# Performance work log

Hardware: AMD Instinct MI355X
Metric: run time of the kernel (lower is better)

Reference implementation:

```python
import jax, jax.numpy as jnp
import numpy as np

WS = 8          # attention window size
NUM_HEADS = 4
PATCH_RATIO = 2 # ratio between consecutive pyramid levels
SCALES = 3


def _rel_idx(ws):
    ch = np.arange(ws)
    coords = np.stack(np.meshgrid(ch, ch, indexing='ij')).reshape(2, -1)
    rel = (coords[:, :, None] - coords[:, None, :]).transpose(1, 2, 0)
    rel[:, :, 0] += ws - 1
    rel[:, :, 1] += ws - 1
    rel[:, :, 0] *= 2 * ws - 1
    return jnp.asarray(rel.sum(-1))  # [ws*ws, ws*ws] int

REL_IDX = _rel_idx(WS)


def win_part(x, ws):
    B, H, W, C = x.shape
    x = x.reshape(B, H // ws, ws, W // ws, ws, C).transpose(0, 1, 3, 2, 4, 5)
    return x.reshape(-1, ws, ws, C)


def win_rev(w, ws, B, H, W):
    C = w.shape[-1]
    x = w.reshape(B, H // ws, W // ws, ws, ws, C).transpose(0, 1, 3, 2, 4, 5)
    return x.reshape(B, H, W, C)


def cross_attn(xw, yw, mw, qw, qb, kw, kb, vw, vb, pw, pb, table):
    # xw, yw: [Bn, N, C]; mw: [Bn, N] overexposure mask
    Bn, N, C = xw.shape
    hd = C // NUM_HEADS
    scale = hd ** -0.5
    q = (xw @ qw.T + qb).reshape(Bn, N, NUM_HEADS, hd).transpose(0, 2, 1, 3) * scale
    k = (yw @ kw.T + kb).reshape(Bn, N, NUM_HEADS, hd).transpose(0, 2, 1, 3)
    v = (yw @ vw.T + vb).reshape(Bn, N, NUM_HEADS, hd).transpose(0, 2, 1, 3)
    attn = jnp.einsum('bhnd,bhmd->bhnm', q, k)
    mask_attn = mw[:, None, :] * mw[:, :, None]          # [Bn, N, N]
    attn = attn * mask_attn[:, None]                     # multiplicative exposure mask
    bias = table[REL_IDX]                                # [N, N, heads]
    attn = attn + bias.transpose(2, 0, 1)[None]
    attn = jax.nn.softmax(attn, axis=-1)
    out = jnp.einsum('bhnm,bhmd->bhnd', attn, v).transpose(0, 2, 1, 3).reshape(Bn, N, C)
    out = out @ pw.T + pb
    return out, attn


def align_level(x, y, params):
    # x, y: [B, H, W, C]; shift_size = 0 (module default)
    B, H, W, C = x.shape
    mask = jnp.where(x > 0.95, 0.0, 1.0).mean(-1, keepdims=True)  # [B,H,W,1]
    x = x * mask
    xw = win_part(x, WS).reshape(-1, WS * WS, C)
    yw = win_part(y, WS).reshape(-1, WS * WS, C)
    mw = win_part(mask, WS).reshape(-1, WS * WS)
    out, attn = cross_attn(xw, yw, mw, *params)
    out = win_rev(out.reshape(-1, WS, WS, C), WS, B, H, W)
    return out, attn


def atttransfer(ta, att, pr):
    # ta: [B, H, W, C] at finer level; att: [nW, heads, WS^2, WS^2] from coarser level
    B, H, W, C = ta.shape
    ws = WS * pr
    w = win_part(ta, ws)                                  # [nW, ws, ws, C]
    nW = w.shape[0]
    w = w.reshape(nW, WS, pr, WS, pr, C).transpose(0, 1, 3, 2, 4, 5)
    w = w.reshape(nW, WS * WS, pr * pr * C)
    out = att.mean(axis=1) @ w                            # [nW, WS^2, pr^2*C]
    out = out.reshape(nW, WS, WS, pr, pr, C).transpose(0, 1, 3, 2, 4, 5).reshape(nW, ws, ws, C)
    return win_rev(out, ws, B, H, W)


def conv3(x, w, b):
    y = jax.lax.conv_general_dilated(x, w, (1, 1), 'SAME',
                                     dimension_numbers=('NCHW', 'OIHW', 'NCHW'))
    return y + b[None, :, None, None]


def lrelu(x):
    return jax.nn.leaky_relu(x, 0.1)


def _forward(ref1, ref2, ref3, ta1, ta2, ta3, q_w, q_b, k_w, k_b, v_w, v_b,
             p_w, p_b, bias_table, fc_w, fc_b):
    refs = [ref1, ref2, ref3]
    tas = [ta1, ta2, ta3]
    upsample_feat = None
    last_att = None
    feat = None
    for i in range(SCALES, 0, -1):
        j = i - 1
        ref = refs[j].transpose(0, 2, 3, 1)   # NCHW -> NHWC
        ta = tas[j].transpose(0, 2, 3, 1)
        params = (q_w[j], q_b[j], k_w[j], k_b[j], v_w[j], v_b[j],
                  p_w[j], p_b[j], bias_table[j])
        aligned, att = align_level(ref, ta, params)
        feat = aligned.transpose(0, 3, 1, 2)  # NHWC -> NCHW
        if i < SCALES:
            atrans = atttransfer(ta, last_att, PATCH_RATIO).transpose(0, 3, 1, 2)
            feat = conv3(jnp.concatenate([feat, upsample_feat, atrans], axis=1),
                         fc_w[j], fc_b[j])
        if i > 1:
            feat = lrelu(feat)
            B, C, Hh, Ww = feat.shape
            upsample_feat = jax.image.resize(feat, (B, C, Hh * 2, Ww * 2), method='bilinear')
        last_att = att
    return lrelu(feat)


def setup_inputs() -> dict:
    key = jax.random.key(0)
    ks = jax.random.split(key, 20)
    B, C = 4, 64
    d = {}
    d['ref1'] = jax.random.normal(ks[0], (B, C, 256, 256), jnp.float32)
    d['ref2'] = jax.random.normal(ks[1], (B, C, 128, 128), jnp.float32)
    d['ref3'] = jax.random.normal(ks[2], (B, C, 64, 64), jnp.float32)
    d['ta1'] = jax.random.normal(ks[3], (B, C, 256, 256), jnp.float32)
    d['ta2'] = jax.random.normal(ks[4], (B, C, 128, 128), jnp.float32)
    d['ta3'] = jax.random.normal(ks[5], (B, C, 64, 64), jnp.float32)
    d['q_w'] = jax.random.normal(ks[6], (3, C, C), jnp.float32) * 0.02
    d['q_b'] = jax.random.normal(ks[7], (3, C), jnp.float32) * 0.02
    d['k_w'] = jax.random.normal(ks[8], (3, C, C), jnp.float32) * 0.02
    d['k_b'] = jax.random.normal(ks[9], (3, C), jnp.float32) * 0.02
    d['v_w'] = jax.random.normal(ks[10], (3, C, C), jnp.float32) * 0.02
    d['v_b'] = jax.random.normal(ks[11], (3, C), jnp.float32) * 0.02
    d['p_w'] = jax.random.normal(ks[12], (3, C, C), jnp.float32) * 0.02
    d['p_b'] = jax.random.normal(ks[13], (3, C), jnp.float32) * 0.02
    d['bias_table'] = jax.random.normal(ks[14], (3, (2 * WS - 1) ** 2, NUM_HEADS), jnp.float32) * 0.02
    d['fc_w'] = jax.random.normal(ks[15], (2, C, 3 * C, 3, 3), jnp.float32) * 0.02
    d['fc_b'] = jax.random.normal(ks[16], (2, C), jnp.float32) * 0.02
    return d


def reference(ref1, ref2, ref3, ta1, ta2, ta3, q_w, q_b, k_w, k_b, v_w, v_b,
              p_w, p_b, bias_table, fc_w, fc_b):
    return _forward(ref1, ref2, ref3, ta1, ta2, ta3, q_w, q_b, k_w, k_b,
                    v_w, v_b, p_w, p_b, bias_table, fc_w, fc_b)
```

## Files before the change

kernel.cpp:

```cpp
#include <hip/hip_runtime.h>
#include <hip/hip_bf16.h>
#include <math.h>

#define LRELU(v) ((v) >= 0.f ? (v) : 0.1f * (v))
#define LOG2E 1.4426950408889634f

typedef __attribute__((ext_vector_type(8))) short short8;
typedef __attribute__((ext_vector_type(4))) float f32x4;

#define MFMA16 __builtin_amdgcn_mfma_f32_16x16x32_bf16

__device__ __forceinline__ float loadf(const float* p) { return *p; }
__device__ __forceinline__ float loadf(const __hip_bfloat16* p) { return __bfloat162float(*p); }
__device__ __forceinline__ short f2bfbits(float f) {
    __hip_bfloat16 h = __float2bfloat16(f);
    return *reinterpret_cast<short*>(&h);
}
__device__ __forceinline__ float bits2f(unsigned short u) {
    union { unsigned int i; float f; } x; x.i = ((unsigned int)u) << 16; return x.f;
}

__global__ __launch_bounds__(256) void nhwc_kernel(const float* __restrict__ ref,
                                                   const float* __restrict__ ta,
                                                   __hip_bfloat16* __restrict__ refn,
                                                   __hip_bfloat16* __restrict__ tan,
                                                   float* __restrict__ maskp,
                                                   int H, int HW) {
    __shared__ float S[2][64][67];
    const int tid = threadIdx.x;
    const int tile = blockIdx.x;
    const int b = blockIdx.y;
    const int tpr = H >> 6;
    const int y = tile / tpr;
    const int x0 = (tile - y * tpr) << 6;
    const size_t ibase = (size_t)b * 64 * HW + (size_t)y * H + x0;

    for (int r = tid; r < 8192; r += 256) {
        int which = r >> 12;
        int c = (r >> 6) & 63;
        int x = r & 63;
        S[which][c][x] = (which ? ta : ref)[ibase + (size_t)c * HW + x];
    }
    __syncthreads();
    if (tid < 64) {
        float s = 0.f;
#pragma unroll
        for (int c = 0; c < 64; ++c) s += (S[0][c][tid] > 0.95f) ? 0.f : 1.f;
        maskp[(size_t)b * HW + (size_t)y * H + x0 + tid] = s * (1.f / 64.f);
    }
    const size_t obase = ((size_t)b * HW + (size_t)y * H + x0) * 64;
    for (int r = tid; r < 8192; r += 256) {
        int which = r >> 12;
        int x = (r >> 6) & 63;
        int c = r & 63;
        (which ? tan : refn)[obase + (size_t)x * 64 + c] = __float2bfloat16(S[which][c][x]);
    }
}

template <bool HASATT>
__global__ __launch_bounds__(256, 4) void fused_attn_kernel(
    const __hip_bfloat16* __restrict__ refn,
    const __hip_bfloat16* __restrict__ tan,
    const float* __restrict__ maskp,
    const __hip_bfloat16* __restrict__ WQ,
    const __hip_bfloat16* __restrict__ WK,
    const __hip_bfloat16* __restrict__ WV,
    const __hip_bfloat16* __restrict__ WPp,
    const float* __restrict__ qb, const float* __restrict__ kb,
    const float* __restrict__ vb, const float* __restrict__ pb,
    const float* __restrict__ btab,
    __hip_bfloat16* __restrict__ aligned,
    __hip_bfloat16* __restrict__ attm,
    int H, int nWx, int nWin)
{
    __shared__ __align__(16) unsigned short PP[64 * 72];
    __shared__ __align__(16) unsigned short KH[64 * 72];
    __shared__ __align__(16) unsigned short VT[64 * 72];
    __shared__ unsigned short BLB[900];
    __shared__ float MSK[64];

    const int HW = H * H;
    const int win = blockIdx.x;
    const int bb = blockIdx.y;
    const int wy = win / nWx, wx = win - wy * nWx;
    const int y0 = wy * 8, x0 = wx * 8;
    const int tid = threadIdx.x;
    const int w = __builtin_amdgcn_readfirstlane(tid >> 6);
    const int l = tid & 63;
    const int lq = l >> 4, lm = l & 15;

    for (int r = tid; r < 900; r += 256)
        BLB[r] = (unsigned short)f2bfbits(btab[r] * LOG2E);
    if (tid < 64)
        MSK[tid] = maskp[(size_t)bb * HW + (size_t)(y0 + (tid >> 3)) * H + x0 + (tid & 7)];

    const int tokr = 16 * w + lm;
    const size_t prow = ((size_t)bb * HW
                         + (size_t)(y0 + (tokr >> 3)) * H + (x0 + (tokr & 7))) * 64;
    const unsigned short* xp = (const unsigned short*)refn + prow;
    const unsigned short* yp = (const unsigned short*)tan + prow;

    f32x4 aq[4], ak[4], av[4];
#pragma unroll
    for (int nt = 0; nt < 4; ++nt) {
        aq[nt] = (f32x4){0.f, 0.f, 0.f, 0.f};
        ak[nt] = (f32x4){0.f, 0.f, 0.f, 0.f};
        av[nt] = (f32x4){0.f, 0.f, 0.f, 0.f};
    }

#pragma unroll
    for (int stage = 0; stage < 2; ++stage) {
        const int cio = stage * 32 + lq * 8;
        short8 xa = *reinterpret_cast<const short8*>(xp + cio);
        short8 ya = *reinterpret_cast<const short8*>(yp + cio);
#pragma unroll
        for (int nt = 0; nt < 4; ++nt) {
            const int co = nt * 16 + lm;
            short8 bq = *reinterpret_cast<const short8*>(WQ + co * 64 + cio);
            aq[nt] = MFMA16(xa, bq, aq[nt], 0, 0, 0);
            short8 bk = *reinterpret_cast<const short8*>(WK + co * 64 + cio);
            ak[nt] = MFMA16(ya, bk, ak[nt], 0, 0, 0);
            short8 bv8 = *reinterpret_cast<const short8*>(WV + co * 64 + cio);
            av[nt] = MFMA16(ya, bv8, av[nt], 0, 0, 0);
        }
    }

#pragma unroll
    for (int nt = 0; nt < 4; ++nt) {
        const int co = nt * 16 + lm;
        const float kbv = kb[co], vbv = vb[co];
#pragma unroll
        for (int r = 0; r < 4; ++r) {
            const int tr = 16 * w + lq * 4 + r;
            const int pr = 16 * (2 * (tr >> 5) + ((tr >> 2) & 1))
                         + 4 * ((tr >> 3) & 3) + (tr & 3);
            KH[pr * 72 + co] = (unsigned short)f2bfbits(ak[nt][r] + kbv);
            VT[co * 72 + tr] = (unsigned short)f2bfbits(av[nt][r] + vbv);
        }
    }
    {
        float mq_r[4];
#pragma unroll
        for (int r = 0; r < 4; ++r) mq_r[r] = MSK[16 * w + lq * 4 + r];
#pragma unroll
        for (int nt = 0; nt < 4; ++nt) {
            const float qbv = qb[nt * 16 + lm];
#pragma unroll
            for (int r = 0; r < 4; ++r)
                PP[(16 * w + lq * 4 + r) * 72 + nt * 16 + lm] =
                    (unsigned short)f2bfbits((aq[nt][r] * mq_r[r] + qbv) * 0.25f);
        }
    }
    __syncthreads();

    const short8 z8 = (short8){0, 0, 0, 0, 0, 0, 0, 0};
    const f32x4 zf = (f32x4){0.f, 0.f, 0.f, 0.f};
    short8 qfrag[4];
#pragma unroll
    for (int h = 0; h < 4; ++h)
        qfrag[h] = (lq < 2)
            ? *reinterpret_cast<const short8*>(&PP[(16 * w + lm) * 72 + 16 * h + lq * 8])
            : z8;

    const float mql = MSK[16 * w + lm] * LOG2E;
    float mkb[4][4];
    int ktab[4][4];
#pragma unroll
    for (int nt = 0; nt < 4; ++nt)
#pragma unroll
        for (int r = 0; r < 4; ++r) {
            int kt = (nt >> 1) * 32 + lq * 8 + (nt & 1) * 4 + r;
            ktab[nt][r] = kt;
            mkb[nt][r] = MSK[kt];
        }
    const int qt = 16 * w + lm;
    const int qi = qt >> 3, qj = qt & 7;

    float attAcc[HASATT ? 4 : 1][HASATT ? 4 : 1];
    if constexpr (HASATT) {
#pragma unroll
        for (int nt = 0; nt < 4; ++nt)
#pragma unroll
            for (int r = 0; r < 4; ++r) attAcc[nt][r] = 0.f;
    }
    f32x4 oacc[4];

#pragma unroll
    for (int hp = 0; hp < 2; ++hp) {
        f32x4 s[2][4];
#pragma unroll
        for (int u = 0; u < 2; ++u) {
            const int h = hp * 2 + u;
#pragma unroll
            for (int nt = 0; nt < 4; ++nt) {
                short8 kf = (lq < 2)
                    ? *reinterpret_cast<const short8*>(
                          &KH[(nt * 16 + lm) * 72 + 16 * h + lq * 8])
                    : z8;
                s[u][nt] = MFMA16(kf, qfrag[h], zf, 0, 0, 0);
            }
        }

        float p[2][4][4];
#pragma unroll
        for (int u = 0; u < 2; ++u) {
            const int h = hp * 2 + u;
#pragma unroll
            for (int nt = 0; nt < 4; ++nt)
#pragma unroll
                for (int r = 0; r < 4; ++r) {
                    int kt = ktab[nt][r];
                    int bidx = (qi - (kt >> 3) + 7) * 15 + (qj - (kt & 7) + 7);
                    p[u][nt][r] = s[u][nt][r] * mql * mkb[nt][r]
                                  + bits2f(BLB[bidx * 4 + h]);
                }
        }
        float mx[2], sum[2];
#pragma unroll
        for (int u = 0; u < 2; ++u) {
            float m = p[u][0][0];
#pragma unroll
            for (int nt = 0; nt < 4; ++nt)
#pragma unroll
                for (int r = 0; r < 4; ++r) m = fmaxf(m, p[u][nt][r]);
            m = fmaxf(m, __shfl_xor(m, 16));
            m = fmaxf(m, __shfl_xor(m, 32));
            mx[u] = m;
        }
#pragma unroll
        for (int u = 0; u < 2; ++u) {
            float sm = 0.f;
#pragma unroll
            for (int nt = 0; nt < 4; ++nt)
#pragma unroll
                for (int r = 0; r < 4; ++r) {
                    p[u][nt][r] = exp2f(p[u][nt][r] - mx[u]);
                    sm += p[u][nt][r];
                }
            sm += __shfl_xor(sm, 16);
            sm += __shfl_xor(sm, 32);
            sum[u] = sm;
        }
#pragma unroll
        for (int u = 0; u < 2; ++u) {
            float inv = 1.f / sum[u];
#pragma unroll
            for (int nt = 0; nt < 4; ++nt)
#pragma unroll
                for (int r = 0; r < 4; ++r) p[u][nt][r] *= inv;
        }

        if constexpr (HASATT) {
#pragma unroll
            for (int u = 0; u < 2; ++u)
#pragma unroll
                for (int nt = 0; nt < 4; ++nt)
#pragma unroll
                    for (int r = 0; r < 4; ++r) attAcc[nt][r] += 0.25f * p[u][nt][r];
        }

#pragma unroll
        for (int u = 0; u < 2; ++u) {
            const int h = hp * 2 + u;
            short8 pb0, pb1;
#pragma unroll
            for (int j = 0; j < 8; ++j) {
                pb0[j] = f2bfbits(p[u][(j >> 2)][j & 3]);
                pb1[j] = f2bfbits(p[u][2 + (j >> 2)][j & 3]);
            }
            short8 vt0 = *reinterpret_cast<const short8*>(&VT[(16 * h + lm) * 72 + lq * 8]);
            short8 vt1 = *reinterpret_cast<const short8*>(&VT[(16 * h + lm) * 72 + 32 + lq * 8]);
            f32x4 o = MFMA16(vt0, pb0, zf, 0, 0, 0);
            o = MFMA16(vt1, pb1, o, 0, 0, 0);
            oacc[h] = o;
        }
    }

    if constexpr (HASATT) {
#pragma unroll
        for (int nt = 0; nt < 4; ++nt)
#pragma unroll
            for (int r = 0; r < 4; ++r)
                PP[(16 * w + lm) * 72 + ktab[nt][r]] =
                    (unsigned short)f2bfbits(attAcc[nt][r]);
        const int rr = 16 * w + (l >> 2), cb = (l & 3) * 16;
        short8 a0 = *reinterpret_cast<const short8*>(&PP[rr * 72 + cb]);
        short8 a1 = *reinterpret_cast<const short8*>(&PP[rr * 72 + cb + 8]);
        unsigned short* gp = (unsigned short*)attm
            + ((size_t)bb * nWin + win) * 4096 + (size_t)rr * 64 + cb;
        *reinterpret_cast<short8*>(gp) = a0;
        *reinterpret_cast<short8*>(gp + 8) = a1;
    }

    short8 oa0, oa1;
#pragma unroll
    for (int j = 0; j < 8; ++j) {
        oa0[j] = f2bfbits(oacc[(j >> 2)][j & 3]);
        oa1[j] = f2bfbits(oacc[2 + (j >> 2)][j & 3]);
    }
    f32x4 eo[4];
#pragma unroll
    for (int nt = 0; nt < 4; ++nt) {
        const int co = nt * 16 + lm;
        short8 wb0 = *reinterpret_cast<const short8*>(WPp + co * 64 + lq * 8);
        short8 wb1 = *reinterpret_cast<const short8*>(WPp + co * 64 + 32 + lq * 8);
        eo[nt] = MFMA16(oa0, wb0, zf, 0, 0, 0);
        eo[nt] = MFMA16(oa1, wb1, eo[nt], 0, 0, 0);
    }
    const size_t obase = (size_t)bb * HW * 64;
#pragma unroll
    for (int nt = 0; nt < 4; ++nt) {
        float pbv = pb[nt * 16 + lm];
#pragma unroll
        for (int r = 0; r < 4; ++r) {
            int tok = 16 * w + lq * 4 + r;
            aligned[obase + ((size_t)(y0 + (tok >> 3)) * H + (x0 + (tok & 7))) * 64
                    + nt * 16 + lm] = __float2bfloat16(eo[nt][r] + pbv);
        }
    }
}

__global__ __launch_bounds__(256) void wsplit_kernel(const float* __restrict__ qw,
                                                     const float* __restrict__ kw,
                                                     const float* __restrict__ vw,
                                                     const float* __restrict__ pw,
                                                     __hip_bfloat16* __restrict__ dst) {
    int idx = blockIdx.x * 256 + threadIdx.x;
    int e = idx & 4095;
    int mat = (idx >> 12) & 3;
    int j = idx >> 14;
    int co = e >> 6, ci = e & 63;
    int src_ci = ci;
    if (mat == 3)
        src_ci = 16 * (2 * (ci >> 5) + ((ci >> 2) & 1)) + 4 * ((ci >> 3) & 3) + (ci & 3);
    const float* src = (mat == 0 ? qw : mat == 1 ? kw : mat == 2 ? vw : pw) + j * 4096;
    float v = src[co * 64 + src_ci];
    __hip_bfloat16 h = __float2bfloat16(v);
    dst[((size_t)j * 4 + mat) * 8192 + e] = h;
    dst[((size_t)j * 4 + mat) * 8192 + 4096 + e] = __float2bfloat16(v - __bfloat162float(h));
}

#define PSTR 4624
__global__ __launch_bounds__(256) void atttrans_kernel(
    const __hip_bfloat16* __restrict__ tan,
    const __hip_bfloat16* __restrict__ attm,
    __hip_bfloat16* __restrict__ outw,
    int H, int HW, int nWx16)
{
    __shared__ __align__(16) unsigned short AT[4608];
    __shared__ __align__(16) unsigned short VTP[4 * PSTR];

    const int tid = threadIdx.x;
    const int win = blockIdx.x;
    const int b = blockIdx.y;
    const int wh = win / nWx16, ww = win - wh * nWx16;
    const int w = __builtin_amdgcn_readfirstlane(tid >> 6);
    const int l = tid & 63;
    const int lq = l >> 4, lm = l & 15;

    const unsigned short* ap = (const unsigned short*)attm
        + ((size_t)b * nWx16 * nWx16 + win) * 4096;
    for (int s = tid; s < 512; s += 256) {
        short8 v = *reinterpret_cast<const short8*>(ap + s * 8);
        *reinterpret_cast<short8*>(&AT[(s >> 3) * 72 + (s & 7) * 8]) = v;
    }

    {
        const int yy = tid >> 4, xx = tid & 15;
        const int pp = ((yy & 1) << 1) | (xx & 1);
        const int s = ((yy >> 1) << 3) | (xx >> 1);
        const unsigned short* tp = (const unsigned short*)tan
            + ((size_t)b * HW + (size_t)(wh * 16 + yy) * H + (ww * 16 + xx)) * 64;
        unsigned short* vbp = &VTP[pp * PSTR + s];
#pragma unroll
        for (int oct = 0; oct < 8; ++oct) {
            short8 v = *reinterpret_cast<const short8*>(tp + oct * 8);
#pragma unroll
            for (int i = 0; i < 8; ++i) vbp[(oct * 8 + i) * 72] = (unsigned short)v[i];
        }
    }
    __syncthreads();

    f32x4 acc[4][4];
#pragma unroll
    for (int pp = 0; pp < 4; ++pp)
#pragma unroll
        for (int nt = 0; nt < 4; ++nt) acc[pp][nt] = (f32x4){0.f, 0.f, 0.f, 0.f};

#pragma unroll
    for (int kk = 0; kk < 2; ++kk) {
        short8 aA = *reinterpret_cast<const short8*>(
                        &AT[(16 * w + lm) * 72 + kk * 32 + lq * 8]);
#pragma unroll
        for (int pp = 0; pp < 4; ++pp) {
#pragma unroll
            for (int nt = 0; nt < 4; ++nt) {
                short8 bB = *reinterpret_cast<const short8*>(
                    &VTP[pp * PSTR + (nt * 16 + lm) * 72 + kk * 32 + lq * 8]);
                acc[pp][nt] = MFMA16(aA, bB, acc[pp][nt], 0, 0, 0);
            }
        }
    }

#pragma unroll
    for (int pp = 0; pp < 4; ++pp) {
        const int pi = pp >> 1, pj = pp & 1;
#pragma unroll
        for (int r = 0; r < 4; ++r) {
            const int t = 16 * w + lq * 4 + r;
            const int Y = wh * 16 + ((t >> 3) << 1) + pi;
            const int X = ww * 16 + ((t & 7) << 1) + pj;
            __hip_bfloat16* op = outw + ((size_t)b * HW + (size_t)Y * H + X) * 64;
#pragma unroll
            for (int nt = 0; nt < 4; ++nt)
                op[nt * 16 + lm] = __float2bfloat16(acc[pp][nt][r]);
        }
    }
}

__global__ __launch_bounds__(256) void wtrans_kernel(const float* __restrict__ src,
                                                     __hip_bfloat16* __restrict__ WH,
                                                     __hip_bfloat16* __restrict__ WL) {
    int idx = blockIdx.x * 256 + threadIdx.x;
    int j = idx & 7;
    int t1 = idx >> 3;
    int co = t1 & 63;
    int t2 = t1 >> 6;
    int oct = t2 & 3;
    int t3 = t2 >> 2;
    int chunk = t3 % 6;
    int kykx = t3 / 6;
    int ci = chunk * 32 + oct * 8 + j;
    int ky = kykx / 3, kx = kykx % 3;
    float v = src[((co * 192 + ci) * 3 + ky) * 3 + kx];
    __hip_bfloat16 h = __float2bfloat16(v);
    WH[idx] = h;
    WL[idx] = __float2bfloat16(v - __bfloat162float(h));
}

__global__ __launch_bounds__(256) void conv_mfma_kernel(
    const __hip_bfloat16* __restrict__ s0, const __hip_bfloat16* __restrict__ s1,
    const __hip_bfloat16* __restrict__ s2,
    const __hip_bfloat16* __restrict__ WHp,
    const float* __restrict__ bias,
    float* __restrict__ out,
    int H, int HW, int mode)
{
    __shared__ short I[6][66][40];

    const int tid = threadIdx.x;
    const int w   = tid >> 6;
    const int l   = tid & 63;
    const int lq  = l >> 4;
    const int lm  = l & 15;
    const int x0  = blockIdx.x * 64;
    const int y0  = blockIdx.y * 4;
    const size_t zoff = (size_t)blockIdx.z * HW * 64;

    f32x4 acc[4][4];
#pragma unroll
    for (int mt = 0; mt < 4; ++mt)
#pragma unroll
        for (int nt = 0; nt < 4; ++nt) acc[mt][nt] = (f32x4){0.f, 0.f, 0.f, 0.f};

    const short8* WH8 = reinterpret_cast<const short8*>(WHp);

    for (int chunk = 0; chunk < 6; ++chunk) {
        __syncthreads();
        const unsigned short* src = reinterpret_cast<const unsigned short*>(
            (chunk < 2) ? s0 : (chunk < 4) ? s1 : s2);
        const int cib = (chunk & 1) * 32;
        for (int s = tid; s < 1584; s += 256) {
            int oct = s & 3;
            int xr = s >> 2;
            int xi = xr % 66;
            int r = xr / 66;
            int gx = x0 - 1 + xi, gy = y0 - 1 + r;
            short8 v = (short8){0, 0, 0, 0, 0, 0, 0, 0};
            if (gx >= 0 && gx < H && gy >= 0 && gy < H)
                v = *reinterpret_cast<const short8*>(
                        src + zoff + ((size_t)gy * H + gx) * 64 + cib + oct * 8);
            *reinterpret_cast<short8*>(&I[r][xi][oct * 8]) = v;
        }
        __syncthreads();

#pragma unroll
        for (int kk = 0; kk < 9; ++kk) {
            const int ky = kk / 3, kx = kk % 3;
            const int wbase = ((kk * 6 + chunk) * 4 + lq) * 64 + lm;
            short8 ah[4];
#pragma unroll
            for (int mt = 0; mt < 4; ++mt) ah[mt] = WH8[wbase + mt * 16];
#pragma unroll
            for (int nt = 0; nt < 4; ++nt) {
                short8 bfrag = *reinterpret_cast<const short8*>(
                                   &I[w + ky][nt * 16 + lm + kx][lq * 8]);
#pragma unroll
                for (int mt = 0; mt < 4; ++mt)
                    acc[mt][nt] = MFMA16(ah[mt], bfrag, acc[mt][nt], 0, 0, 0);
            }
        }
    }

    const int y = y0 + w;
#pragma unroll
    for (int mt = 0; mt < 4; ++mt) {
#pragma unroll
        for (int r = 0; r < 4; ++r) {
            const int co = mt * 16 + lq * 4 + r;
            const float bv = bias[co];
#pragma unroll
            for (int nt = 0; nt < 4; ++nt) {
                float v = acc[mt][nt][r] + bv;
                const int x = x0 + nt * 16 + lm;
                if (mode == 0) {
                    v = LRELU(v);
                    out[zoff + (size_t)co * HW + (size_t)y * H + x] = v;
                } else {
                    out[zoff + ((size_t)y * H + x) * 64 + co] = v;
                }
            }
        }
    }
}

template <typename T>
__global__ __launch_bounds__(256) void upsample_kernel(const T* __restrict__ in,
                                                       __hip_bfloat16* __restrict__ out,
                                                       int Hin, int total) {
    int idx = blockIdx.x * 256 + threadIdx.x;
    if (idx >= total) return;
    int c = idx & 63;
    int r1 = idx >> 6;
    int W2 = Hin * 2;
    int X = r1 % W2;
    int r2 = r1 / W2;
    int Y = r2 % W2;
    int b = r2 / W2;
    int y0 = Y >> 1, x0 = X >> 1;
    int ya = (Y & 1) ? y0 + 1 : y0 - 1;
    int xa = (X & 1) ? x0 + 1 : x0 - 1;
    ya = ya < 0 ? 0 : (ya >= Hin ? Hin - 1 : ya);
    xa = xa < 0 ? 0 : (xa >= Hin ? Hin - 1 : xa);
    const T* p = in + (size_t)b * Hin * Hin * 64;
    float v00 = LRELU(loadf(p + ((size_t)y0 * Hin + x0) * 64 + c));
    float v01 = LRELU(loadf(p + ((size_t)y0 * Hin + xa) * 64 + c));
    float v10 = LRELU(loadf(p + ((size_t)ya * Hin + x0) * 64 + c));
    float v11 = LRELU(loadf(p + ((size_t)ya * Hin + xa) * 64 + c));
    out[idx] = __float2bfloat16(0.5625f * v00 + 0.1875f * (v01 + v10) + 0.0625f * v11);
}

extern "C" void kernel_launch(void* const* d_in, const int* in_sizes, int n_in,
                              void* d_out, int out_size, void* d_ws, size_t ws_size,
                              hipStream_t stream) {
    const float* refs[3] = { (const float*)d_in[0], (const float*)d_in[1], (const float*)d_in[2] };
    const float* tas[3]  = { (const float*)d_in[3], (const float*)d_in[4], (const float*)d_in[5] };
    const float* q_w = (const float*)d_in[6];
    const float* q_b = (const float*)d_in[7];
    const float* k_w = (const float*)d_in[8];
    const float* k_b = (const float*)d_in[9];
    const float* v_w = (const float*)d_in[10];
    const float* v_b = (const float*)d_in[11];
    const float* p_w = (const float*)d_in[12];
    const float* p_b = (const float*)d_in[13];
    const float* btab = (const float*)d_in[14];
    const float* fc_w = (const float*)d_in[15];
    const float* fc_b = (const float*)d_in[16];

    const size_t WBYTES = 4ull * 221184 + 196608;
    const size_t BIG4 = 4ull * 65536 * 64 * 2;
    const size_t NEED4 = WBYTES + 4 * BIG4 + 4ull * 65536 * 4 + 4096;
    const int NB = (ws_size >= NEED4) ? 4 : 1;
    const size_t BIG = (size_t)NB * 65536 * 64 * 2;

    char* p = (char*)d_ws;
    __hip_bfloat16* WH0 = (__hip_bfloat16*)p;  p += 221184;
    __hip_bfloat16* WL0 = (__hip_bfloat16*)p;  p += 221184;
    __hip_bfloat16* WH1 = (__hip_bfloat16*)p;  p += 221184;
    __hip_bfloat16* WL1 = (__hip_bfloat16*)p;  p += 221184;
    __hip_bfloat16* WTA = (__hip_bfloat16*)p;  p += 196608;
    __hip_bfloat16* XRN = (__hip_bfloat16*)p;  p += BIG;
    __hip_bfloat16* XTN = (__hip_bfloat16*)p;  p += BIG;
    __hip_bfloat16* ALIGNED = (__hip_bfloat16*)p;  p += BIG;
    __hip_bfloat16* UPS     = (__hip_bfloat16*)p;  p += BIG;
    float* MASKP = (float*)p;  p += (size_t)NB * 65536 * 4;
    __hip_bfloat16* ATRANS = XRN;
    __hip_bfloat16 *ATTMA, *ATTMB;
    float* FEAT2;
    if (NB == 4) {
        ATTMA = (__hip_bfloat16*)d_out;
        ATTMB = (__hip_bfloat16*)((float*)d_out + 1048576);
        FEAT2 = (float*)d_out + 5242880;
    } else {
        ATTMA = (__hip_bfloat16*)p;  p += (size_t)64 * 4096 * 2;
        ATTMB = (__hip_bfloat16*)p;  p += (size_t)256 * 4096 * 2;
        FEAT2 = (float*)p;           p += (size_t)16384 * 64 * 4;
    }

    wtrans_kernel<<<432, 256, 0, stream>>>(fc_w, WH0, WL0);
    wtrans_kernel<<<432, 256, 0, stream>>>(fc_w + 110592, WH1, WL1);
    wsplit_kernel<<<192, 256, 0, stream>>>(q_w, k_w, v_w, p_w, WTA);

    for (int b0 = 0; b0 < 4; b0 += NB) {
        const float* ref1 = refs[0] + (size_t)b0 * 64 * 65536;
        const float* ta1  = tas[0]  + (size_t)b0 * 64 * 65536;
        const float* ref2 = refs[1] + (size_t)b0 * 64 * 16384;
        const float* ta2  = tas[1]  + (size_t)b0 * 64 * 16384;
        const float* ref3 = refs[2] + (size_t)b0 * 64 * 4096;
        const float* ta3  = tas[2]  + (size_t)b0 * 64 * 4096;

        nhwc_kernel<<<dim3(64, NB), 256, 0, stream>>>(ref3, ta3, XRN, XTN, MASKP, 64, 4096);
        fused_attn_kernel<true><<<dim3(64, NB), 256, 0, stream>>>(
            XRN, XTN, MASKP,
            WTA + (2*4+0)*8192, WTA + (2*4+1)*8192, WTA + (2*4+2)*8192, WTA + (2*4+3)*8192,
            q_b + 2*64, k_b + 2*64, v_b + 2*64, p_b + 2*64,
            btab + 2*900, ALIGNED, ATTMA, 64, 8, 64);
        upsample_kernel<__hip_bfloat16><<<(NB * 64 * 16384) / 256, 256, 0, stream>>>(
            ALIGNED, UPS, 64, NB * 64 * 16384);

        nhwc_kernel<<<dim3(256, NB), 256, 0, stream>>>(ref2, ta2, XRN, XTN, MASKP, 128, 16384);
        fused_attn_kernel<true><<<dim3(256, NB), 256, 0, stream>>>(
            XRN, XTN, MASKP,
            WTA + (1*4+0)*8192, WTA + (1*4+1)*8192, WTA + (1*4+2)*8192, WTA + (1*4+3)*8192,
            q_b + 64, k_b + 64, v_b + 64, p_b + 64,
            btab + 900, ALIGNED, ATTMB, 128, 16, 256);
        atttrans_kernel<<<dim3(64, NB), 256, 0, stream>>>(
            XTN, ATTMA, ATRANS, 128, 16384, 8);
        conv_mfma_kernel<<<dim3(2, 32, NB), 256, 0, stream>>>(
            ALIGNED, UPS, ATRANS, WH1, fc_b + 64, FEAT2, 128, 16384, 1);
        upsample_kernel<float><<<(NB * 64 * 65536) / 256, 256, 0, stream>>>(
            FEAT2, UPS, 128, NB * 64 * 65536);

        nhwc_kernel<<<dim3(1024, NB), 256, 0, stream>>>(ref1, ta1, XRN, XTN, MASKP, 256, 65536);
        fused_attn_kernel<false><<<dim3(1024, NB), 256, 0, stream>>>(
            XRN, XTN, MASKP,
            WTA + 0*8192, WTA + 1*8192, WTA + 2*8192, WTA + 3*8192,
            q_b, k_b, v_b, p_b,
            btab, ALIGNED, nullptr, 256, 32, 1024);
        atttrans_kernel<<<dim3(256, NB), 256, 0, stream>>>(
            XTN, ATTMB, ATRANS, 256, 65536, 16);
        conv_mfma_kernel<<<dim3(4, 64, NB), 256, 0, stream>>>(
            ALIGNED, UPS, ATRANS, WH0, fc_b,
            (float*)d_out + (size_t)b0 * 64 * 65536, 256, 65536, 0);
    }
}
```

Before: 431.2 us.

## Prefetch next conv input chunk into registers while computing current chunk

```diff
diff --git a/kernel.cpp b/kernel.cpp
--- a/kernel.cpp
+++ b/kernel.cpp
@@ -456,6 +456,7 @@
     const int x0  = blockIdx.x * 64;
     const int y0  = blockIdx.y * 4;
     const size_t zoff = (size_t)blockIdx.z * HW * 64;
+    const short8 z8 = (short8){0, 0, 0, 0, 0, 0, 0, 0};
 
     f32x4 acc[4][4];
 #pragma unroll
@@ -465,25 +466,51 @@
 
     const short8* WH8 = reinterpret_cast<const short8*>(WHp);
 
+    short8 st[7];
+    const unsigned short* b0 = (const unsigned short*)s0;
+    const unsigned short* b1 = (const unsigned short*)s1;
+    const unsigned short* b2 = (const unsigned short*)s2;
+
+    auto stage_load = [&](int chunk) {
+        const unsigned short* src = (chunk < 2) ? b0 : (chunk < 4) ? b1 : b2;
+        const int cib = (chunk & 1) * 32;
+#pragma unroll
+        for (int s = 0; s < 7; ++s) {
+            int slot = tid + (s << 8);
+            if (slot < 1584) {
+                int oct = slot & 3;
+                int xr = slot >> 2;
+                int xi = xr % 66;
+                int r = xr / 66;
+                int gx = x0 - 1 + xi, gy = y0 - 1 + r;
+                short8 v = z8;
+                if (gx >= 0 && gx < H && gy >= 0 && gy < H)
+                    v = *reinterpret_cast<const short8*>(
+                            src + zoff + ((size_t)gy * H + gx) * 64 + cib + oct * 8);
+                st[s] = v;
+            }
+        }
+    };
+    auto stage_write = [&]() {
+#pragma unroll
+        for (int s = 0; s < 7; ++s) {
+            int slot = tid + (s << 8);
+            if (slot < 1584) {
+                int oct = slot & 3;
+                int xr = slot >> 2;
+                int xi = xr % 66;
+                int r = xr / 66;
+                *reinterpret_cast<short8*>(&I[r][xi][oct * 8]) = st[s];
+            }
+        }
+    };
+
+    stage_load(0);
+    stage_write();
+    __syncthreads();
+
     for (int chunk = 0; chunk < 6; ++chunk) {
-        __syncthreads();
-        const unsigned short* src = reinterpret_cast<const unsigned short*>(
-            (chunk < 2) ? s0 : (chunk < 4) ? s1 : s2);
-        const int cib = (chunk & 1) * 32;
-        for (int s = tid; s < 1584; s += 256) {
-            int oct = s & 3;
-            int xr = s >> 2;
-            int xi = xr % 66;
-            int r = xr / 66;
-            int gx = x0 - 1 + xi, gy = y0 - 1 + r;
-            short8 v = (short8){0, 0, 0, 0, 0, 0, 0, 0};
-            if (gx >= 0 && gx < H && gy >= 0 && gy < H)
-                v = *reinterpret_cast<const short8*>(
-                        src + zoff + ((size_t)gy * H + gx) * 64 + cib + oct * 8);
-            *reinterpret_cast<short8*>(&I[r][xi][oct * 8]) = v;
-        }
-        __syncthreads();
-
+        if (chunk < 5) stage_load(chunk + 1);
 #pragma unroll
         for (int kk = 0; kk < 9; ++kk) {
             const int ky = kk / 3, kx = kk % 3;
@@ -499,6 +526,11 @@
                 for (int mt = 0; mt < 4; ++mt)
                     acc[mt][nt] = MFMA16(ah[mt], bfrag, acc[mt][nt], 0, 0, 0);
             }
+        }
+        if (chunk < 5) {
+            __syncthreads();
+            stage_write();
+            __syncthreads();
         }
     }
 
```

After: 407.6 us. -5.5%, faster.
